# Optimization experiments

Hardware: AMD Instinct MI355X
Metric: run time of the kernel (lower is better)

Reference implementation:

```python
import jax, jax.numpy as jnp
import numpy as np

L, H, E, D, FF, V, CTX = 8, 16, 1024, 64, 4096, 2048, 2048
B, T = 4, 1024


def _ln(x, g, b, eps=1e-5):
    mu = x.mean(-1, keepdims=True)
    var = ((x - mu) ** 2).mean(-1, keepdims=True)
    return (x - mu) * jax.lax.rsqrt(var + eps) * g + b


def setup_inputs() -> dict:
    key = jax.random.key(0)
    ks = jax.random.split(key, 12)
    s = 0.02
    return {
        "tokens": jax.random.randint(ks[0], (B, T), 0, V),
        "tok_emb": jax.random.normal(ks[1], (V, E), jnp.float32) * s,
        "pos_emb": jax.random.normal(ks[2], (CTX, E), jnp.float32) * s,
        "Wq": jax.random.normal(ks[3], (L, H, E, D), jnp.float32) * s,
        "Wk": jax.random.normal(ks[4], (L, H, E, D), jnp.float32) * s,
        "Wv": jax.random.normal(ks[5], (L, H, E, D), jnp.float32) * s,
        "Wo": jax.random.normal(ks[6], (L, H * D, E), jnp.float32) * s,
        "bo": jnp.zeros((L, E), jnp.float32),
        "ln1_g": jnp.ones((L, E), jnp.float32),
        "ln1_b": jnp.zeros((L, E), jnp.float32),
        "ln2_g": jnp.ones((L, E), jnp.float32),
        "ln2_b": jnp.zeros((L, E), jnp.float32),
        "W1": jax.random.normal(ks[7], (L, E, FF), jnp.float32) * s,
        "b1": jnp.zeros((L, FF), jnp.float32),
        "W2": jax.random.normal(ks[8], (L, FF, E), jnp.float32) * s,
        "b2": jnp.zeros((L, E), jnp.float32),
        "lnf_g": jnp.ones((E,), jnp.float32),
        "lnf_b": jnp.zeros((E,), jnp.float32),
        "Wlm": jax.random.normal(ks[9], (E, V), jnp.float32) * s,
        "blm": jnp.zeros((V,), jnp.float32),
    }


def reference(tokens, tok_emb, pos_emb, Wq, Wk, Wv, Wo, bo, ln1_g, ln1_b,
              ln2_g, ln2_b, W1, b1, W2, b2, lnf_g, lnf_b, Wlm, blm):
    # NOTE: original indexes pos_embd with token ids (pos_embd(x.int()))
    x = tok_emb[tokens] + pos_emb[tokens]  # [B,T,E]
    t = x.shape[1]
    causal = jnp.tril(jnp.ones((t, t), bool))
    scale = 1.0 / jnp.sqrt(jnp.float32(D))
    for l in range(L):
        x = _ln(x, ln1_g[l], ln1_b[l])
        q = jnp.einsum('bte,hed->bhtd', x, Wq[l])
        k = jnp.einsum('bte,hed->bhtd', x, Wk[l])
        v = jnp.einsum('bte,hed->bhtd', x, Wv[l])
        scores = jnp.einsum('bhtd,bhsd->bhts', q, k) * scale
        scores = jnp.where(causal, scores, -jnp.inf)
        att = jax.nn.softmax(scores, axis=-1)
        o = jnp.einsum('bhts,bhsd->bhtd', att, v)
        o = o.transpose(0, 2, 1, 3).reshape(x.shape[0], t, H * D)
        x = x + o @ Wo[l] + bo[l]
        x = _ln(x, ln2_g[l], ln2_b[l])
        x = x + jax.nn.relu(x @ W1[l] + b1[l]) @ W2[l] + b2[l]
    x = _ln(x, lnf_g, lnf_b)
    return x @ Wlm + blm
```

## Files before the change

kernel.cpp:

```cpp
#include <hip/hip_runtime.h>
#include <hip/hip_bf16.h>

#define LAYERS 8
#define H_ 16
#define E_ 1024
#define D_ 64
#define FF_ 4096
#define V_ 2048
#define B_ 4
#define T_ 1024
#define MTOK (B_*T_)

typedef __bf16 bf16x8_t __attribute__((ext_vector_type(8)));
typedef __bf16 bf16x4_t __attribute__((ext_vector_type(4)));
typedef float f32x4_t __attribute__((ext_vector_type(4)));
typedef __hip_bfloat16 bf16_t;

__device__ __forceinline__ bf16_t f2b(float f) { return __float2bfloat16(f); }

__global__ void embed_kernel(const int* __restrict__ tokens,
                             const float* __restrict__ te,
                             const float* __restrict__ pe,
                             bf16_t* __restrict__ x) {
  int row = blockIdx.x;
  int tok = tokens[row];
  int t = threadIdx.x;
  float4 va = ((const float4*)(te + (size_t)tok * E_))[t];
  float4 vp = ((const float4*)(pe + (size_t)tok * E_))[t];
  bf16x4_t o;
  o[0] = (__bf16)(va.x + vp.x); o[1] = (__bf16)(va.y + vp.y);
  o[2] = (__bf16)(va.z + vp.z); o[3] = (__bf16)(va.w + vp.w);
  ((bf16x4_t*)(x + (size_t)row * E_))[t] = o;
}

__global__ __launch_bounds__(256) void ln_kernel(const bf16_t* __restrict__ xin,
                                                 bf16_t* __restrict__ xout,
                                                 const float* __restrict__ g,
                                                 const float* __restrict__ b) {
  int row = blockIdx.x, tid = threadIdx.x;
  bf16x4_t v4 = ((const bf16x4_t*)(xin + (size_t)row * E_))[tid];
  float v0 = (float)v4[0], v1 = (float)v4[1], v2 = (float)v4[2], v3 = (float)v4[3];
  float s  = v0 + v1 + v2 + v3;
  float sq = v0*v0 + v1*v1 + v2*v2 + v3*v3;
  for (int off = 32; off; off >>= 1) {
    s  += __shfl_xor(s, off, 64);
    sq += __shfl_xor(sq, off, 64);
  }
  __shared__ float2 wred[4];
  if ((tid & 63) == 0) wred[tid >> 6] = make_float2(s, sq);
  __syncthreads();
  float2 w0 = wred[0], w1 = wred[1], w2 = wred[2], w3 = wred[3];
  float S = w0.x + w1.x + w2.x + w3.x, SQ = w0.y + w1.y + w2.y + w3.y;
  float mean = S * (1.0f / E_);
  float var  = SQ * (1.0f / E_) - mean * mean;
  float inv = rsqrtf(var + 1e-5f);
  float4 gv = ((const float4*)g)[tid];
  float4 bv = ((const float4*)b)[tid];
  bf16x4_t o;
  o[0] = (__bf16)((v0 - mean) * inv * gv.x + bv.x);
  o[1] = (__bf16)((v1 - mean) * inv * gv.y + bv.y);
  o[2] = (__bf16)((v2 - mean) * inv * gv.z + bv.z);
  o[3] = (__bf16)((v3 - mean) * inv * gv.w + bv.w);
  ((bf16x4_t*)(xout + (size_t)row * E_))[tid] = o;
}

__global__ __launch_bounds__(256) void reduce_ln_kernel(
    const bf16_t* __restrict__ p,
    const bf16_t* __restrict__ tin,
    const float* __restrict__ bias,
    bf16_t* __restrict__ r,
    bf16_t* __restrict__ tout,
    const float* __restrict__ g,
    const float* __restrict__ b) {
  int row = blockIdx.x, tid = threadIdx.x;
  size_t base = (size_t)row * E_ + tid * 4;
  bf16x4_t tv = *(const bf16x4_t*)(tin + base);
  bf16x4_t p0 = *(const bf16x4_t*)(p + base);
  bf16x4_t p1 = *(const bf16x4_t*)(p + (size_t)MTOK * E_ + base);
  float4 bv = ((const float4*)bias)[tid];
  float y0 = (float)tv[0] + (float)p0[0] + (float)p1[0] + bv.x;
  float y1 = (float)tv[1] + (float)p0[1] + (float)p1[1] + bv.y;
  float y2 = (float)tv[2] + (float)p0[2] + (float)p1[2] + bv.z;
  float y3 = (float)tv[3] + (float)p0[3] + (float)p1[3] + bv.w;
  bf16x4_t rv;
  rv[0] = (__bf16)y0; rv[1] = (__bf16)y1; rv[2] = (__bf16)y2; rv[3] = (__bf16)y3;
  *(bf16x4_t*)(r + base) = rv;
  float z0 = (float)rv[0], z1 = (float)rv[1], z2 = (float)rv[2], z3 = (float)rv[3];
  float s = z0 + z1 + z2 + z3, sq = z0*z0 + z1*z1 + z2*z2 + z3*z3;
  for (int off = 32; off; off >>= 1) {
    s  += __shfl_xor(s, off, 64);
    sq += __shfl_xor(sq, off, 64);
  }
  __shared__ float2 wred[4];
  if ((tid & 63) == 0) wred[tid >> 6] = make_float2(s, sq);
  __syncthreads();
  float2 w0 = wred[0], w1 = wred[1], w2 = wred[2], w3 = wred[3];
  float S = w0.x + w1.x + w2.x + w3.x, SQ = w0.y + w1.y + w2.y + w3.y;
  float mean = S * (1.0f / E_);
  float var  = SQ * (1.0f / E_) - mean * mean;
  float inv = rsqrtf(var + 1e-5f);
  float4 gv = ((const float4*)g)[tid];
  float4 b2v = ((const float4*)b)[tid];
  bf16x4_t o;
  o[0] = (__bf16)((z0 - mean) * inv * gv.x + b2v.x);
  o[1] = (__bf16)((z1 - mean) * inv * gv.y + b2v.y);
  o[2] = (__bf16)((z2 - mean) * inv * gv.z + b2v.z);
  o[3] = (__bf16)((z3 - mean) * inv * gv.w + b2v.w);
  *(bf16x4_t*)(tout + base) = o;
}

__global__ void prep_weights_kernel(const float* __restrict__ Wq,
                                    const float* __restrict__ Wk,
                                    const float* __restrict__ Wv,
                                    const float* __restrict__ Wo,
                                    const float* __restrict__ W1,
                                    const float* __restrict__ W2,
                                    bf16_t* __restrict__ WqkvT,
                                    bf16_t* __restrict__ WoT,
                                    bf16_t* __restrict__ W1T,
                                    bf16_t* __restrict__ W2T,
                                    int l) {
  __shared__ float tile[32][33];
  int bid = blockIdx.x;
  const float* src; bf16_t* dst; int R, C, r0, c0;
  if (bid < 3072) {
    int op = bid >> 10, rem = bid & 1023;
    int h = rem >> 6, tt = rem & 63;
    const float* W = (op == 0) ? Wq : (op == 1) ? Wk : Wv;
    src = W + (size_t)l * H_ * E_ * D_ + (size_t)h * E_ * D_;
    dst = WqkvT + (size_t)op * E_ * H_ * D_ + (size_t)h * E_ * D_;
    R = E_; C = D_; r0 = (tt >> 1) * 32; c0 = (tt & 1) * 32;
  } else if (bid < 4096) {
    int tt = bid - 3072;
    src = Wo + (size_t)l * H_ * D_ * E_; dst = WoT;
    R = H_ * D_; C = E_; r0 = (tt >> 5) * 32; c0 = (tt & 31) * 32;
  } else if (bid < 8192) {
    int tt = bid - 4096;
    src = W1 + (size_t)l * E_ * FF_; dst = W1T;
    R = E_; C = FF_; r0 = (tt >> 7) * 32; c0 = (tt & 127) * 32;
  } else {
    int tt = bid - 8192;
    src = W2 + (size_t)l * FF_ * E_; dst = W2T;
    R = FF_; C = E_; r0 = (tt >> 5) * 32; c0 = (tt & 31) * 32;
  }
  int tx = threadIdx.x, ty = threadIdx.y;
  for (int i = 0; i < 4; i++)
    tile[ty + i * 8][tx] = src[(size_t)(r0 + ty + i * 8) * C + (c0 + tx)];
  __syncthreads();
  for (int i = 0; i < 4; i++)
    dst[(size_t)(c0 + ty + i * 8) * R + (r0 + tx)] = f2b(tile[tx][ty + i * 8]);
}

__global__ void transpose_kernel(const float* __restrict__ in, bf16_t* __restrict__ out,
                                 int R, int C) {
  __shared__ float tile[32][33];
  int r0 = blockIdx.y * 32, c0 = blockIdx.x * 32;
  int tx = threadIdx.x, ty = threadIdx.y;
  for (int i = 0; i < 4; i++)
    tile[ty + i * 8][tx] = in[(size_t)(r0 + ty + i * 8) * C + (c0 + tx)];
  __syncthreads();
  for (int i = 0; i < 4; i++)
    out[(size_t)(c0 + ty + i * 8) * R + (r0 + tx)] = f2b(tile[tx][ty + i * 8]);
}

enum { MODE_F32 = 0, MODE_BF16 = 1, MODE_QKV = 2, MODE_BF16R = 3 };

__device__ __forceinline__ void gload16(const bf16_t* g, bf16_t* l) {
  __builtin_amdgcn_global_load_lds((const __attribute__((address_space(1))) void*)g,
                                   (__attribute__((address_space(3))) void*)l, 16, 0, 0);
}

__device__ __forceinline__ int2 xcd_tile(int gx, int chm, int chn) {
  int flat = blockIdx.y * gx + blockIdx.x;
  int xcd = flat & 7, j = flat >> 3;
  int cpr = gx / chn;
  int cr = xcd / cpr, cc = xcd - cr * cpr;
  int jm = j / chn, jn = j - jm * chn;
  return make_int2(cr * chm + jm, cc * chn + jn);
}

#define BK 32
template <int BM, int BN, int MODE>
__global__ __launch_bounds__(256) void gemm97_kernel(
    const bf16_t* __restrict__ A, long long sAz, int lda,
    const bf16_t* __restrict__ Bt, long long sBz, int ldb,
    void* __restrict__ C, long long sCz,
    const float* __restrict__ bias,
    const void* __restrict__ resid,
    int M, int N, int K, int relu, int chm, int chn) {
  constexpr int FR = BM / 32, FC = BN / 32;
  constexpr int A_ISS = BM / 64, B_ISS = BN / 64;
  __shared__ __align__(16) bf16_t As[2][BM * BK];
  __shared__ __align__(16) bf16_t Bs[2][BN * BK];
  int tid = threadIdx.x;
  int z = blockIdx.z;
  int2 mn = xcd_tile(gridDim.x, chm, chn);
  int m0 = mn.x * BM, n0 = mn.y * BN;
  const bf16_t* Ab = A + (size_t)z * sAz + (size_t)m0 * lda;
  const bf16_t* Bb = Bt + (size_t)z * sBz + (size_t)n0 * ldb;
  int lane = tid & 63, wave = tid >> 6;
  int wr = (wave >> 1) * (BM / 2), wc = (wave & 1) * (BN / 2);
  int lr = lane & 15, lk = (lane >> 4) * 8;
  int srow = tid >> 2;
  int scol = (tid & 3) * 8;

  f32x4_t acc[FR][FC];
  for (int i = 0; i < FR; i++)
    for (int j = 0; j < FC; j++)
      acc[i][j] = (f32x4_t){0.f, 0.f, 0.f, 0.f};

  auto stage = [&](int buf, int k0) {
#pragma unroll
    for (int i = 0; i < A_ISS; i++)
      gload16(Ab + (size_t)(i * 64 + srow) * lda + k0 + scol, &As[buf][i * 2048 + wave * 512]);
#pragma unroll
    for (int i = 0; i < B_ISS; i++)
      gload16(Bb + (size_t)(i * 64 + srow) * ldb + k0 + scol, &Bs[buf][i * 2048 + wave * 512]);
  };

  int nk = K / BK;
  stage(0, 0);
  __syncthreads();
  int cur = 0;
  for (int kt = 0; kt < nk; ++kt) {
    if (kt + 1 < nk) stage(cur ^ 1, (kt + 1) * BK);
    bf16x8_t af[FR], bfv[FC];
#pragma unroll
    for (int i = 0; i < FR; i++)
      af[i] = *(const bf16x8_t*)(&As[cur][(wr + i * 16 + lr) * BK + lk]);
#pragma unroll
    for (int j = 0; j < FC; j++)
      bfv[j] = *(const bf16x8_t*)(&Bs[cur][(wc + j * 16 + lr) * BK + lk]);
#pragma unroll
    for (int i = 0; i < FR; i++)
#pragma unroll
      for (int j = 0; j < FC; j++)
        acc[i][j] = __builtin_amdgcn_mfma_f32_16x16x32_bf16(af[i], bfv[j], acc[i][j], 0, 0, 0);
    __syncthreads();
    cur ^= 1;
  }

#pragma unroll
  for (int i = 0; i < FR; i++)
#pragma unroll
    for (int j = 0; j < FC; j++) {
      f32x4_t v = acc[i][j];
      int n = n0 + wc + j * 16 + lr;
      int mb = m0 + wr + i * 16 + (lane >> 4) * 4;
#pragma unroll
      for (int r = 0; r < 4; r++) {
        int m = mb + r;
        float val = v[r];
        if (bias) val += bias[n];
        if (relu) val = fmaxf(val, 0.f);
        if (MODE == MODE_F32) {
          size_t idx = (size_t)z * sCz + (size_t)m * N + n;
          ((float*)C)[idx] = val;
        } else if (MODE == MODE_BF16) {
          size_t idx = (size_t)z * sCz + (size_t)m * N + n;
          ((bf16_t*)C)[idx] = f2b(val);
        } else if (MODE == MODE_BF16R) {
          size_t idx = (size_t)m * N + n;
          val += __bfloat162float(((const bf16_t*)resid)[idx]);
          ((bf16_t*)C)[idx] = f2b(val);
        } else {
          int sect = n >> 10, hd = n & 1023, h = hd >> 6, d = hd & 63;
          int b = m >> 10, t = m & 1023;
          size_t base = (size_t)sect * ((size_t)B_ * H_ * T_ * D_);
          size_t idx = base + ((size_t)(b * H_ + h) << 16) +
                       (sect == 2 ? (size_t)((d << 10) + t) : (size_t)((t << 6) + d));
          ((bf16_t*)C)[idx] = f2b(val);
        }
      }
    }
}

template <int MODE>
__global__ __launch_bounds__(512) void gemm3_kernel(
    const bf16_t* __restrict__ A, int lda,
    const bf16_t* __restrict__ Bt, int ldb,
    void* __restrict__ C, long long sCz,
    const float* __restrict__ bias,
    int M, int N, int kspan, int relu, int chm, int chn) {
  constexpr int ABUFE = 256 * 64;
  constexpr int BBUFE = 128 * 64;
  __shared__ __align__(16) bf16_t LA[3 * ABUFE];
  __shared__ __align__(16) bf16_t LB[3 * BBUFE];
  int tid = threadIdx.x, lane = tid & 63, wave = tid >> 6;
  int wm = wave >> 1, wn = wave & 1;
  int z = blockIdx.z;
  int2 mn = xcd_tile(gridDim.x, chm, chn);
  int m0 = mn.x * 256, n0 = mn.y * 128;
  const bf16_t* Ab = A + (size_t)m0 * lda + (size_t)z * kspan;
  const bf16_t* Bb = Bt + (size_t)n0 * ldb + (size_t)z * kspan;
  int sr = lane & 15, sc = (lane >> 4) * 8;

  f32x4_t acc[4][4];
#pragma unroll
  for (int i = 0; i < 4; i++)
#pragma unroll
    for (int j = 0; j < 4; j++)
      acc[i][j] = (f32x4_t){0.f, 0.f, 0.f, 0.f};

  auto stageh = [&](int b, int kt, int h) {
    int kg = kt * 64;
#pragma unroll
    for (int ch = 0; ch < 2; ch++) {
      int sub = wave * 4 + 2 * h + ch;
      gload16(Ab + (size_t)((sub >> 1) * 16 + sr) * lda + kg + (sub & 1) * 32 + sc,
              LA + b * ABUFE + sub * 512);
    }
    {
      int sub = wave * 2 + h;
      gload16(Bb + (size_t)((sub >> 1) * 16 + sr) * ldb + kg + (sub & 1) * 32 + sc,
              LB + b * BBUFE + sub * 512);
    }
  };

  auto phase = [&](int b, int ks, int t, int nk) {
    bf16x8_t af[4], bfv[4];
    unsigned abase = (unsigned)(size_t)(LA + b * ABUFE);
    unsigned bbase = (unsigned)(size_t)(LB + b * BBUFE);
#pragma unroll
    for (int i = 0; i < 4; i++) {
      unsigned ad = abase + (unsigned)((((wm * 4 + i) * 2 + ks) * 512 + lane * 8) * 2);
      asm volatile("ds_read_b128 %0, %1" : "=v"(af[i]) : "v"(ad));
    }
#pragma unroll
    for (int j = 0; j < 4; j++) {
      unsigned bd = bbase + (unsigned)((((wn * 4 + j) * 2 + ks) * 512 + lane * 8) * 2);
      asm volatile("ds_read_b128 %0, %1" : "=v"(bfv[j]) : "v"(bd));
    }
    if (t + 2 < nk) stageh((t + 2) % 3, t + 2, ks);
    __builtin_amdgcn_s_barrier();
    asm volatile("s_waitcnt lgkmcnt(0)" ::: "memory");
    __builtin_amdgcn_sched_barrier(0);
    __builtin_amdgcn_s_setprio(1);
#pragma unroll
    for (int i = 0; i < 4; i++)
#pragma unroll
      for (int j = 0; j < 4; j++)
        acc[i][j] = __builtin_amdgcn_mfma_f32_16x16x32_bf16(af[i], bfv[j], acc[i][j], 0, 0, 0);
    __builtin_amdgcn_s_setprio(0);
  };

  int nk = kspan / 64;
  stageh(0, 0, 0); stageh(0, 0, 1);
  stageh(1, 1, 0); stageh(1, 1, 1);
  for (int t = 0; t < nk; ++t) {
    int b = t % 3;
    if (t + 1 < nk) { asm volatile("s_waitcnt vmcnt(6)" ::: "memory"); }
    else            { asm volatile("s_waitcnt vmcnt(0)" ::: "memory"); }
    __builtin_amdgcn_s_barrier();
    phase(b, 0, t, nk);
    phase(b, 1, t, nk);
  }

#pragma unroll
  for (int i = 0; i < 4; i++)
#pragma unroll
    for (int j = 0; j < 4; j++) {
      f32x4_t v = acc[i][j];
      int n = n0 + wn * 64 + j * 16 + (lane & 15);
      int mb = m0 + wm * 64 + i * 16 + (lane >> 4) * 4;
#pragma unroll
      for (int r = 0; r < 4; r++) {
        int m = mb + r;
        float val = v[r];
        if (bias) val += bias[n];
        if (relu) val = fmaxf(val, 0.f);
        if (MODE == MODE_F32) {
          size_t idx = (size_t)z * sCz + (size_t)m * N + n;
          ((float*)C)[idx] = val;
        } else {
          size_t idx = (size_t)z * sCz + (size_t)m * N + n;
          ((bf16_t*)C)[idx] = f2b(val);
        }
      }
    }
}

#define KPAD 72

__global__ __launch_bounds__(256) void flash_kernel(
    const bf16_t* __restrict__ q,
    const bf16_t* __restrict__ kk,
    const bf16_t* __restrict__ vt,
    bf16_t* __restrict__ o) {
  __shared__ __align__(16) bf16_t Ks[64 * KPAD];
  __shared__ __align__(16) bf16_t Vs[64 * KPAD];
  __shared__ __align__(16) bf16_t Ps[4][16 * KPAD];
  int bid = blockIdx.x;
  int qi = 15 - (bid >> 6);
  int bh = bid & 63;
  int b = bh >> 4, h = bh & 15;
  const bf16_t* qb = q + ((size_t)bh << 16);
  const bf16_t* kb = kk + ((size_t)bh << 16);
  const bf16_t* vb = vt + ((size_t)bh << 16);
  int tid = threadIdx.x, lane = tid & 63, wave = tid >> 6;
  int lr = lane & 15, lg = lane >> 4;
  int qbase = qi * 64;

  bf16x8_t qf[2];
  {
    const bf16_t* qrow = qb + (size_t)(qbase + wave * 16 + lr) * D_ + lg * 8;
    qf[0] = *(const bf16x8_t*)(qrow);
    qf[1] = *(const bf16x8_t*)(qrow + 32);
  }

  float m_r[4], l_r[4];
  f32x4_t oc[4];
#pragma unroll
  for (int r = 0; r < 4; r++) { m_r[r] = -1e30f; l_r[r] = 0.f; }
#pragma unroll
  for (int j = 0; j < 4; j++) oc[j] = (f32x4_t){0.f, 0.f, 0.f, 0.f};

  int srow = tid >> 2, scol = (tid & 3) * 16;

  bf16x8_t k0, k1, v0, v1;
  {
    const bf16_t* kg = kb + (size_t)srow * D_ + scol;
    k0 = *(const bf16x8_t*)kg;
    k1 = *(const bf16x8_t*)(kg + 8);
    const bf16_t* vg = vb + (size_t)srow * T_ + scol;
    v0 = *(const bf16x8_t*)vg;
    v1 = *(const bf16x8_t*)(vg + 8);
  }

  for (int s = 0; s <= qi; s++) {
    __syncthreads();
    *(bf16x8_t*)(&Ks[srow * KPAD + scol]) = k0;
    *(bf16x8_t*)(&Ks[srow * KPAD + scol + 8]) = k1;
    *(bf16x8_t*)(&Vs[srow * KPAD + scol]) = v0;
    *(bf16x8_t*)(&Vs[srow * KPAD + scol + 8]) = v1;
    __syncthreads();

    if (s < qi) {
      int kv1 = (s + 1) * 64;
      const bf16_t* kg = kb + (size_t)(kv1 + srow) * D_ + scol;
      k0 = *(const bf16x8_t*)kg;
      k1 = *(const bf16x8_t*)(kg + 8);
      const bf16_t* vg = vb + (size_t)srow * T_ + kv1 + scol;
      v0 = *(const bf16x8_t*)vg;
      v1 = *(const bf16x8_t*)(vg + 8);
    }

    int kv0 = s * 64;
    f32x4_t sc[4];
#pragma unroll
    for (int j = 0; j < 4; j++) {
      f32x4_t a = (f32x4_t){0.f, 0.f, 0.f, 0.f};
      bf16x8_t b0 = *(const bf16x8_t*)(&Ks[(j * 16 + lr) * KPAD + lg * 8]);
      bf16x8_t b1 = *(const bf16x8_t*)(&Ks[(j * 16 + lr) * KPAD + lg * 8 + 32]);
      a = __builtin_amdgcn_mfma_f32_16x16x32_bf16(qf[0], b0, a, 0, 0, 0);
      a = __builtin_amdgcn_mfma_f32_16x16x32_bf16(qf[1], b1, a, 0, 0, 0);
      sc[j] = a;
    }
    if (s == qi) {
#pragma unroll
      for (int j = 0; j < 4; j++)
#pragma unroll
        for (int r = 0; r < 4; r++) {
          int kvp = kv0 + j * 16 + lr;
          int qp  = qbase + wave * 16 + lg * 4 + r;
          sc[j][r] = (kvp <= qp) ? sc[j][r] * 0.125f : -1e30f;
        }
    } else {
#pragma unroll
      for (int j = 0; j < 4; j++)
#pragma unroll
        for (int r = 0; r < 4; r++) sc[j][r] *= 0.125f;
    }

    float ex[4];
#pragma unroll
    for (int r = 0; r < 4; r++) {
      float v = fmaxf(fmaxf(sc[0][r], sc[1][r]), fmaxf(sc[2][r], sc[3][r]));
      v = fmaxf(v, __shfl_xor(v, 1, 64));
      v = fmaxf(v, __shfl_xor(v, 2, 64));
      v = fmaxf(v, __shfl_xor(v, 4, 64));
      v = fmaxf(v, __shfl_xor(v, 8, 64));
      float mn = fmaxf(m_r[r], v);
      ex[r] = __expf(m_r[r] - mn);
      m_r[r] = mn;
      l_r[r] *= ex[r];
    }
#pragma unroll
    for (int j = 0; j < 4; j++)
#pragma unroll
      for (int r = 0; r < 4; r++) {
        float p = __expf(sc[j][r] - m_r[r]);
        l_r[r] += p;
        Ps[wave][(lg * 4 + r) * KPAD + j * 16 + lr] = f2b(p);
      }

#pragma unroll
    for (int j = 0; j < 4; j++)
#pragma unroll
      for (int r = 0; r < 4; r++) oc[j][r] *= ex[r];

    bf16x8_t pa0 = *(const bf16x8_t*)(&Ps[wave][lr * KPAD + lg * 8]);
    bf16x8_t pa1 = *(const bf16x8_t*)(&Ps[wave][lr * KPAD + lg * 8 + 32]);
#pragma unroll
    for (int j = 0; j < 4; j++) {
      bf16x8_t vb0 = *(const bf16x8_t*)(&Vs[(j * 16 + lr) * KPAD + lg * 8]);
      bf16x8_t vb1 = *(const bf16x8_t*)(&Vs[(j * 16 + lr) * KPAD + lg * 8 + 32]);
      oc[j] = __builtin_amdgcn_mfma_f32_16x16x32_bf16(pa0, vb0, oc[j], 0, 0, 0);
      oc[j] = __builtin_amdgcn_mfma_f32_16x16x32_bf16(pa1, vb1, oc[j], 0, 0, 0);
    }
  }

#pragma unroll
  for (int r = 0; r < 4; r++) {
    float v = l_r[r];
    v += __shfl_xor(v, 1, 64);
    v += __shfl_xor(v, 2, 64);
    v += __shfl_xor(v, 4, 64);
    v += __shfl_xor(v, 8, 64);
    l_r[r] = 1.f / v;
  }
  bf16_t* ob = o + ((size_t)(b * T_ + qbase + wave * 16)) * (H_ * D_) + h * D_;
#pragma unroll
  for (int j = 0; j < 4; j++)
#pragma unroll
    for (int r = 0; r < 4; r++) {
      int qrow = lg * 4 + r;
      ob[(size_t)qrow * (H_ * D_) + j * 16 + lr] = f2b(oc[j][r] * l_r[r]);
    }
}

extern "C" void kernel_launch(void* const* d_in, const int* in_sizes, int n_in,
                              void* d_out, int out_size, void* d_ws, size_t ws_size,
                              hipStream_t stream) {
  (void)in_sizes; (void)n_in; (void)out_size; (void)ws_size;
  const int*   tokens = (const int*)d_in[0];
  const float* tok_emb = (const float*)d_in[1];
  const float* pos_emb = (const float*)d_in[2];
  const float* Wq = (const float*)d_in[3];
  const float* Wk = (const float*)d_in[4];
  const float* Wv = (const float*)d_in[5];
  const float* Wo = (const float*)d_in[6];
  const float* bo = (const float*)d_in[7];
  const float* ln1_g = (const float*)d_in[8];
  const float* ln1_b = (const float*)d_in[9];
  const float* ln2_g = (const float*)d_in[10];
  const float* ln2_b = (const float*)d_in[11];
  const float* W1 = (const float*)d_in[12];
  const float* b1 = (const float*)d_in[13];
  const float* W2 = (const float*)d_in[14];
  const float* b2 = (const float*)d_in[15];
  const float* lnf_g = (const float*)d_in[16];
  const float* lnf_b = (const float*)d_in[17];
  const float* Wlm = (const float*)d_in[18];
  const float* blm = (const float*)d_in[19];

  char* w = (char*)d_ws;
  size_t off = 0;
  auto alloc = [&](size_t bytes) { void* p = (void*)(w + off); off += (bytes + 255) & ~(size_t)255; return p; };
  bf16_t* r    = (bf16_t*)alloc((size_t)MTOK * E_ * 2);
  bf16_t* t    = (bf16_t*)alloc((size_t)MTOK * E_ * 2);
  bf16_t* q    = (bf16_t*)alloc((size_t)B_ * H_ * T_ * D_ * 2);
  bf16_t* kk   = (bf16_t*)alloc((size_t)B_ * H_ * T_ * D_ * 2);
  bf16_t* vt   = (bf16_t*)alloc((size_t)B_ * H_ * T_ * D_ * 2);
  bf16_t* o    = (bf16_t*)alloc((size_t)MTOK * E_ * 2);
  bf16_t* h1   = (bf16_t*)alloc((size_t)MTOK * FF_ * 2);
  bf16_t* WqkvT = (bf16_t*)alloc((size_t)3 * E_ * H_ * D_ * 2);
  bf16_t* WoT  = (bf16_t*)alloc((size_t)E_ * H_ * D_ * 2);
  bf16_t* W1T  = (bf16_t*)alloc((size_t)E_ * FF_ * 2);
  bf16_t* W2T  = (bf16_t*)alloc((size_t)E_ * FF_ * 2);
  bf16_t* WlmT = (bf16_t*)alloc((size_t)E_ * V_ * 2);
  bf16_t* p2   = (bf16_t*)alloc((size_t)2 * MTOK * E_ * 2);

  embed_kernel<<<MTOK, 256, 0, stream>>>(tokens, tok_emb, pos_emb, r);
  transpose_kernel<<<dim3(V_ / 32, E_ / 32), dim3(32, 8), 0, stream>>>(Wlm, WlmT, E_, V_);
  ln_kernel<<<MTOK, 256, 0, stream>>>(r, t, ln1_g, ln1_b);

  for (int l = 0; l < LAYERS; l++) {
    prep_weights_kernel<<<12288, dim3(32, 8), 0, stream>>>(
        Wq, Wk, Wv, Wo, W1, W2, WqkvT, WoT, W1T, W2T, l);

    gemm97_kernel<128, 128, MODE_QKV><<<dim3(24, 32, 1), 256, 0, stream>>>(
        t, 0, E_, WqkvT, 0, E_, q, 0, nullptr, nullptr, MTOK, 3 * H_ * D_, E_, 0, 8, 12);

    flash_kernel<<<1024, 256, 0, stream>>>(q, kk, vt, o);

    gemm97_kernel<128, 128, MODE_BF16R><<<dim3(8, 32, 1), 256, 0, stream>>>(
        o, 0, H_ * D_, WoT, 0, H_ * D_, r, 0, bo + l * E_, t, MTOK, E_, H_ * D_, 0, 4, 8);

    ln_kernel<<<MTOK, 256, 0, stream>>>(r, t, ln2_g + l * E_, ln2_b + l * E_);

    gemm3_kernel<MODE_BF16><<<dim3(32, 16, 1), 512, 0, stream>>>(
        t, E_, W1T, E_, h1, 0, b1 + l * FF_, MTOK, FF_, E_, 1, 8, 8);
    gemm3_kernel<MODE_BF16><<<dim3(8, 16, 2), 512, 0, stream>>>(
        h1, FF_, W2T, FF_, p2, (long long)MTOK * E_, nullptr, MTOK, E_, FF_ / 2, 0, 2, 8);
    const float* gn = (l + 1 < LAYERS) ? (ln1_g + (l + 1) * E_) : lnf_g;
    const float* bn = (l + 1 < LAYERS) ? (ln1_b + (l + 1) * E_) : lnf_b;
    reduce_ln_kernel<<<MTOK, 256, 0, stream>>>(p2, t, b2 + l * E_, r, t, gn, bn);
  }

  gemm3_kernel<MODE_F32><<<dim3(16, 16, 1), 512, 0, stream>>>(
      t, E_, WlmT, E_, d_out, 0, blm, MTOK, V_, E_, 0, 8, 4);
}
```

Before: 2.164 ms.

## Batch weight prep across layers and widen flash attention query tiles

Weight conversion and transposition for all layers now runs in one launch up front when the workspace is large enough, replacing one prep launch per layer. The flash attention kernel now processes 128 query rows per block with 8 waves. Each K/V tile loaded into shared memory is shared by twice as many query rows, and waves skip key tiles that lie entirely past their causal limit. The tradeoff is more workspace and larger blocks with some idle waves near the diagonal.

```diff
diff --git a/kernel.cpp b/kernel.cpp
--- a/kernel.cpp
+++ b/kernel.cpp
@@ -119,28 +119,29 @@
                                     bf16_t* __restrict__ WoT,
                                     bf16_t* __restrict__ W1T,
                                     bf16_t* __restrict__ W2T,
-                                    int l) {
+                                    int l0) {
   __shared__ float tile[32][33];
   int bid = blockIdx.x;
+  int l = l0 + blockIdx.y, dl = blockIdx.y;
   const float* src; bf16_t* dst; int R, C, r0, c0;
   if (bid < 3072) {
     int op = bid >> 10, rem = bid & 1023;
     int h = rem >> 6, tt = rem & 63;
     const float* W = (op == 0) ? Wq : (op == 1) ? Wk : Wv;
     src = W + (size_t)l * H_ * E_ * D_ + (size_t)h * E_ * D_;
-    dst = WqkvT + (size_t)op * E_ * H_ * D_ + (size_t)h * E_ * D_;
+    dst = WqkvT + (size_t)dl * 3 * E_ * H_ * D_ + (size_t)op * E_ * H_ * D_ + (size_t)h * E_ * D_;
     R = E_; C = D_; r0 = (tt >> 1) * 32; c0 = (tt & 1) * 32;
   } else if (bid < 4096) {
     int tt = bid - 3072;
-    src = Wo + (size_t)l * H_ * D_ * E_; dst = WoT;
+    src = Wo + (size_t)l * H_ * D_ * E_; dst = WoT + (size_t)dl * H_ * D_ * E_;
     R = H_ * D_; C = E_; r0 = (tt >> 5) * 32; c0 = (tt & 31) * 32;
   } else if (bid < 8192) {
     int tt = bid - 4096;
-    src = W1 + (size_t)l * E_ * FF_; dst = W1T;
+    src = W1 + (size_t)l * E_ * FF_; dst = W1T + (size_t)dl * E_ * FF_;
     R = E_; C = FF_; r0 = (tt >> 7) * 32; c0 = (tt & 127) * 32;
   } else {
     int tt = bid - 8192;
-    src = W2 + (size_t)l * FF_ * E_; dst = W2T;
+    src = W2 + (size_t)l * FF_ * E_; dst = W2T + (size_t)dl * FF_ * E_;
     R = FF_; C = E_; r0 = (tt >> 5) * 32; c0 = (tt & 31) * 32;
   }
   int tx = threadIdx.x, ty = threadIdx.y;
@@ -382,16 +383,16 @@
 
 #define KPAD 72
 
-__global__ __launch_bounds__(256) void flash_kernel(
+__global__ __launch_bounds__(512) void flash_kernel(
     const bf16_t* __restrict__ q,
     const bf16_t* __restrict__ kk,
     const bf16_t* __restrict__ vt,
     bf16_t* __restrict__ o) {
   __shared__ __align__(16) bf16_t Ks[64 * KPAD];
   __shared__ __align__(16) bf16_t Vs[64 * KPAD];
-  __shared__ __align__(16) bf16_t Ps[4][16 * KPAD];
+  __shared__ __align__(16) bf16_t Ps[8][16 * KPAD];
   int bid = blockIdx.x;
-  int qi = 15 - (bid >> 6);
+  int qt = 7 - (bid >> 6);
   int bh = bid & 63;
   int b = bh >> 4, h = bh & 15;
   const bf16_t* qb = q + ((size_t)bh << 16);
@@ -399,11 +400,12 @@
   const bf16_t* vb = vt + ((size_t)bh << 16);
   int tid = threadIdx.x, lane = tid & 63, wave = tid >> 6;
   int lr = lane & 15, lg = lane >> 4;
-  int qbase = qi * 64;
+  int qbase = qt * 128;
+  int qwlo = qbase + wave * 16;
 
   bf16x8_t qf[2];
   {
-    const bf16_t* qrow = qb + (size_t)(qbase + wave * 16 + lr) * D_ + lg * 8;
+    const bf16_t* qrow = qb + (size_t)(qwlo + lr) * D_ + lg * 8;
     qf[0] = *(const bf16x8_t*)(qrow);
     qf[1] = *(const bf16x8_t*)(qrow + 32);
   }
@@ -415,37 +417,28 @@
 #pragma unroll
   for (int j = 0; j < 4; j++) oc[j] = (f32x4_t){0.f, 0.f, 0.f, 0.f};
 
-  int srow = tid >> 2, scol = (tid & 3) * 16;
-
-  bf16x8_t k0, k1, v0, v1;
-  {
-    const bf16_t* kg = kb + (size_t)srow * D_ + scol;
-    k0 = *(const bf16x8_t*)kg;
-    k1 = *(const bf16x8_t*)(kg + 8);
-    const bf16_t* vg = vb + (size_t)srow * T_ + scol;
-    v0 = *(const bf16x8_t*)vg;
-    v1 = *(const bf16x8_t*)(vg + 8);
-  }
-
-  for (int s = 0; s <= qi; s++) {
+  int srow = tid >> 3, scol = (tid & 7) * 8;
+
+  bf16x8_t k0, v0;
+  k0 = *(const bf16x8_t*)(kb + (size_t)srow * D_ + scol);
+  v0 = *(const bf16x8_t*)(vb + (size_t)srow * T_ + scol);
+
+  int nst = qt * 2 + 2;
+  for (int s = 0; s < nst; s++) {
     __syncthreads();
     *(bf16x8_t*)(&Ks[srow * KPAD + scol]) = k0;
-    *(bf16x8_t*)(&Ks[srow * KPAD + scol + 8]) = k1;
     *(bf16x8_t*)(&Vs[srow * KPAD + scol]) = v0;
-    *(bf16x8_t*)(&Vs[srow * KPAD + scol + 8]) = v1;
     __syncthreads();
 
-    if (s < qi) {
+    if (s + 1 < nst) {
       int kv1 = (s + 1) * 64;
-      const bf16_t* kg = kb + (size_t)(kv1 + srow) * D_ + scol;
-      k0 = *(const bf16x8_t*)kg;
-      k1 = *(const bf16x8_t*)(kg + 8);
-      const bf16_t* vg = vb + (size_t)srow * T_ + kv1 + scol;
-      v0 = *(const bf16x8_t*)vg;
-      v1 = *(const bf16x8_t*)(vg + 8);
+      k0 = *(const bf16x8_t*)(kb + (size_t)(kv1 + srow) * D_ + scol);
+      v0 = *(const bf16x8_t*)(vb + (size_t)srow * T_ + kv1 + scol);
     }
 
     int kv0 = s * 64;
+    if (kv0 > qwlo + 15) continue;
+
     f32x4_t sc[4];
 #pragma unroll
     for (int j = 0; j < 4; j++) {
@@ -456,13 +449,13 @@
       a = __builtin_amdgcn_mfma_f32_16x16x32_bf16(qf[1], b1, a, 0, 0, 0);
       sc[j] = a;
     }
-    if (s == qi) {
+    if (kv0 + 63 > qwlo) {
 #pragma unroll
       for (int j = 0; j < 4; j++)
 #pragma unroll
         for (int r = 0; r < 4; r++) {
           int kvp = kv0 + j * 16 + lr;
-          int qp  = qbase + wave * 16 + lg * 4 + r;
+          int qp  = qwlo + lg * 4 + r;
           sc[j][r] = (kvp <= qp) ? sc[j][r] * 0.125f : -1e30f;
         }
     } else {
@@ -519,7 +512,7 @@
     v += __shfl_xor(v, 8, 64);
     l_r[r] = 1.f / v;
   }
-  bf16_t* ob = o + ((size_t)(b * T_ + qbase + wave * 16)) * (H_ * D_) + h * D_;
+  bf16_t* ob = o + ((size_t)(b * T_ + qwlo)) * (H_ * D_) + h * D_;
 #pragma unroll
   for (int j = 0; j < 4; j++)
 #pragma unroll
@@ -532,7 +525,7 @@
 extern "C" void kernel_launch(void* const* d_in, const int* in_sizes, int n_in,
                               void* d_out, int out_size, void* d_ws, size_t ws_size,
                               hipStream_t stream) {
-  (void)in_sizes; (void)n_in; (void)out_size; (void)ws_size;
+  (void)in_sizes; (void)n_in; (void)out_size;
   const int*   tokens = (const int*)d_in[0];
   const float* tok_emb = (const float*)d_in[1];
   const float* pos_emb = (const float*)d_in[2];
@@ -564,35 +557,52 @@
   bf16_t* vt   = (bf16_t*)alloc((size_t)B_ * H_ * T_ * D_ * 2);
   bf16_t* o    = (bf16_t*)alloc((size_t)MTOK * E_ * 2);
   bf16_t* h1   = (bf16_t*)alloc((size_t)MTOK * FF_ * 2);
-  bf16_t* WqkvT = (bf16_t*)alloc((size_t)3 * E_ * H_ * D_ * 2);
-  bf16_t* WoT  = (bf16_t*)alloc((size_t)E_ * H_ * D_ * 2);
-  bf16_t* W1T  = (bf16_t*)alloc((size_t)E_ * FF_ * 2);
-  bf16_t* W2T  = (bf16_t*)alloc((size_t)E_ * FF_ * 2);
   bf16_t* WlmT = (bf16_t*)alloc((size_t)E_ * V_ * 2);
   bf16_t* p2   = (bf16_t*)alloc((size_t)2 * MTOK * E_ * 2);
 
+  size_t wqkv_b = (size_t)3 * E_ * H_ * D_ * 2;
+  size_t wo_b   = (size_t)E_ * H_ * D_ * 2;
+  size_t w1_b   = (size_t)E_ * FF_ * 2;
+  size_t w2_b   = (size_t)FF_ * E_ * 2;
+  size_t per_layer = wqkv_b + wo_b + w1_b + w2_b;
+  bool allw = ws_size > off + (size_t)LAYERS * per_layer + (1 << 22);
+  int nl = allw ? LAYERS : 1;
+  bf16_t* WqkvT = (bf16_t*)alloc(wqkv_b * nl);
+  bf16_t* WoT   = (bf16_t*)alloc(wo_b * nl);
+  bf16_t* W1T   = (bf16_t*)alloc(w1_b * nl);
+  bf16_t* W2T   = (bf16_t*)alloc(w2_b * nl);
+
   embed_kernel<<<MTOK, 256, 0, stream>>>(tokens, tok_emb, pos_emb, r);
   transpose_kernel<<<dim3(V_ / 32, E_ / 32), dim3(32, 8), 0, stream>>>(Wlm, WlmT, E_, V_);
+  if (allw)
+    prep_weights_kernel<<<dim3(12288, LAYERS), dim3(32, 8), 0, stream>>>(
+        Wq, Wk, Wv, Wo, W1, W2, WqkvT, WoT, W1T, W2T, 0);
   ln_kernel<<<MTOK, 256, 0, stream>>>(r, t, ln1_g, ln1_b);
 
   for (int l = 0; l < LAYERS; l++) {
-    prep_weights_kernel<<<12288, dim3(32, 8), 0, stream>>>(
-        Wq, Wk, Wv, Wo, W1, W2, WqkvT, WoT, W1T, W2T, l);
+    if (!allw)
+      prep_weights_kernel<<<dim3(12288, 1), dim3(32, 8), 0, stream>>>(
+          Wq, Wk, Wv, Wo, W1, W2, WqkvT, WoT, W1T, W2T, l);
+    int li = allw ? l : 0;
+    const bf16_t* WqkvT_l = WqkvT + (size_t)li * 3 * E_ * H_ * D_;
+    const bf16_t* WoT_l   = WoT + (size_t)li * E_ * H_ * D_;
+    const bf16_t* W1T_l   = W1T + (size_t)li * E_ * FF_;
+    const bf16_t* W2T_l   = W2T + (size_t)li * FF_ * E_;
 
     gemm97_kernel<128, 128, MODE_QKV><<<dim3(24, 32, 1), 256, 0, stream>>>(
-        t, 0, E_, WqkvT, 0, E_, q, 0, nullptr, nullptr, MTOK, 3 * H_ * D_, E_, 0, 8, 12);
-
-    flash_kernel<<<1024, 256, 0, stream>>>(q, kk, vt, o);
+        t, 0, E_, WqkvT_l, 0, E_, q, 0, nullptr, nullptr, MTOK, 3 * H_ * D_, E_, 0, 8, 12);
+
+    flash_kernel<<<512, 512, 0, stream>>>(q, kk, vt, o);
 
     gemm97_kernel<128, 128, MODE_BF16R><<<dim3(8, 32, 1), 256, 0, stream>>>(
-        o, 0, H_ * D_, WoT, 0, H_ * D_, r, 0, bo + l * E_, t, MTOK, E_, H_ * D_, 0, 4, 8);
+        o, 0, H_ * D_, WoT_l, 0, H_ * D_, r, 0, bo + l * E_, t, MTOK, E_, H_ * D_, 0, 4, 8);
 
     ln_kernel<<<MTOK, 256, 0, stream>>>(r, t, ln2_g + l * E_, ln2_b + l * E_);
 
     gemm3_kernel<MODE_BF16><<<dim3(32, 16, 1), 512, 0, stream>>>(
-        t, E_, W1T, E_, h1, 0, b1 + l * FF_, MTOK, FF_, E_, 1, 8, 8);
+        t, E_, W1T_l, E_, h1, 0, b1 + l * FF_, MTOK, FF_, E_, 1, 8, 8);
     gemm3_kernel<MODE_BF16><<<dim3(8, 16, 2), 512, 0, stream>>>(
-        h1, FF_, W2T, FF_, p2, (long long)MTOK * E_, nullptr, MTOK, E_, FF_ / 2, 0, 2, 8);
+        h1, FF_, W2T_l, FF_, p2, (long long)MTOK * E_, nullptr, MTOK, E_, FF_ / 2, 0, 2, 8);
     const float* gn = (l + 1 < LAYERS) ? (ln1_g + (l + 1) * E_) : lnf_g;
     const float* bn = (l + 1 < LAYERS) ? (ln1_b + (l + 1) * E_) : lnf_b;
     reduce_ln_kernel<<<MTOK, 256, 0, stream>>>(p2, t, b2 + l * E_, r, t, gn, bn);
```

Measured after the change: 2.233 ms (median of 2 runs). 3.2% more time.
